# Performance work log

Measured on AMD Instinct MI355X. Metric: run time of the kernel, lower is better.

## Reference

```python
import jax, jax.numpy as jnp
import numpy as np

CH = 512
GROUPS = 32  # _valid_num_groups(512, 32)
EPS = 1e-6

def setup_inputs() -> dict:
    key = jax.random.key(0)
    ks = jax.random.split(key, 11)
    B, C, H, W = 8, CH, 64, 64
    s = 0.02
    return {
        "x": jax.random.normal(ks[0], (B, C, H, W), jnp.float32),
        "gn_w": jnp.ones((C,), jnp.float32),
        "gn_b": jnp.zeros((C,), jnp.float32),
        "q_w": jax.random.normal(ks[1], (C, C), jnp.float32) * s,
        "q_b": jnp.zeros((C,), jnp.float32),
        "k_w": jax.random.normal(ks[2], (C, C), jnp.float32) * s,
        "k_b": jnp.zeros((C,), jnp.float32),
        "v_w": jax.random.normal(ks[3], (C, C), jnp.float32) * s,
        "v_b": jnp.zeros((C,), jnp.float32),
        "proj_w": jax.random.normal(ks[4], (C, C), jnp.float32) * s,
        "proj_b": jnp.zeros((C,), jnp.float32),
    }

def _group_norm(x, w, b):
    B, C, H, W = x.shape
    g = GROUPS
    xg = x.reshape(B, g, C // g, H, W)
    mu = xg.mean(axis=(2, 3, 4), keepdims=True)
    var = xg.var(axis=(2, 3, 4), keepdims=True)
    xn = ((xg - mu) * jax.lax.rsqrt(var + EPS)).reshape(B, C, H, W)
    return xn * w[None, :, None, None] + b[None, :, None, None]

def _conv1x1(h, w, b):
    # h: [B,C,H,W]; w: [Cout,Cin]; 1x1 conv == channel matmul
    return jnp.einsum('bchw,dc->bdhw', h, w) + b[None, :, None, None]

def reference(x, gn_w, gn_b, q_w, q_b, k_w, k_b, v_w, v_b, proj_w, proj_b):
    B, C, H, W = x.shape
    N = H * W
    h = _group_norm(x, gn_w, gn_b)
    q = _conv1x1(h, q_w, q_b).reshape(B, C, N)  # [B,C,N]
    k = _conv1x1(h, k_w, k_b).reshape(B, C, N)
    v = _conv1x1(h, v_w, v_b).reshape(B, C, N)
    # attn[b,i,j] = sum_c q[b,c,i]*k[b,c,j] scaled
    attn = jnp.einsum('bci,bcj->bij', q, k) * (C ** -0.5)
    attn = jax.nn.softmax(attn, axis=-1)
    # out[b,c,i] = sum_j v[b,c,j]*attn[b,i,j]  (bmm(v, attn^T))
    o = jnp.einsum('bcj,bij->bci', v, attn).reshape(B, C, H, W)
    o = _conv1x1(o, proj_w, proj_b)
    return x + o
```

## Files before the change

kernel.cpp:

```cpp
#include <hip/hip_runtime.h>

typedef unsigned short u16;
typedef __attribute__((ext_vector_type(8))) short short8;
typedef __attribute__((ext_vector_type(4))) float f32x4;

__device__ __forceinline__ u16 f32_to_bf16(float f) {
  unsigned u = __float_as_uint(f);
  u += 0x7fffu + ((u >> 16) & 1u);
  return (u16)(u >> 16);
}
__device__ __forceinline__ float bf16_to_f32(u16 h) {
  return __uint_as_float(((unsigned)h) << 16);
}

#define GLD_LDS16(gp, lp)                                                  \
  __builtin_amdgcn_global_load_lds(                                        \
      (const __attribute__((address_space(1))) void*)(gp),                 \
      (__attribute__((address_space(3))) void*)(lp), 16, 0, 0)

#define WAITVM(n) asm volatile("s_waitcnt vmcnt(" #n ")" ::: "memory")

__device__ __forceinline__ void wg_barrier() {
  asm volatile("" ::: "memory");
  __builtin_amdgcn_s_barrier();
  asm volatile("" ::: "memory");
}

__global__ __launch_bounds__(256) void cvt4_f32_bf16(const float* __restrict__ s0,
                                                     const float* __restrict__ s1,
                                                     const float* __restrict__ s2,
                                                     const float* __restrict__ s3,
                                                     u16* __restrict__ d0,
                                                     u16* __restrict__ d1,
                                                     u16* __restrict__ d2,
                                                     u16* __restrict__ d3) {
  const float* s = blockIdx.y == 0 ? s0 : blockIdx.y == 1 ? s1 : blockIdx.y == 2 ? s2 : s3;
  u16* d = blockIdx.y == 0 ? d0 : blockIdx.y == 1 ? d1 : blockIdx.y == 2 ? d2 : d3;
  int i = blockIdx.x * 256 + threadIdx.x;
  float4 v = ((const float4*)s)[i];
  uint2 r;
  r.x = (unsigned)f32_to_bf16(v.x) | ((unsigned)f32_to_bf16(v.y) << 16);
  r.y = (unsigned)f32_to_bf16(v.z) | ((unsigned)f32_to_bf16(v.w) << 16);
  ((uint2*)d)[i] = r;
}

__global__ __launch_bounds__(1024) void gn_stats(const float* __restrict__ x,
                                                 float2* __restrict__ stats) {
  int bg = blockIdx.x;
  const float* xp = x + (long)bg * 65536;
  int t = threadIdx.x;
  float s = 0.f, ss = 0.f;
  for (int i = t; i < 16384; i += 1024) {
    float4 v = ((const float4*)xp)[i];
    s += (v.x + v.y) + (v.z + v.w);
    ss += (v.x * v.x + v.y * v.y) + (v.z * v.z + v.w * v.w);
  }
#pragma unroll
  for (int o = 32; o; o >>= 1) { s += __shfl_xor(s, o); ss += __shfl_xor(ss, o); }
  __shared__ float rs[16], rq[16];
  int wave = t >> 6, lane = t & 63;
  if (lane == 0) { rs[wave] = s; rq[wave] = ss; }
  __syncthreads();
  if (wave == 0) {
    float a = lane < 16 ? rs[lane] : 0.f;
    float b = lane < 16 ? rq[lane] : 0.f;
#pragma unroll
    for (int o = 8; o; o >>= 1) { a += __shfl_xor(a, o); b += __shfl_xor(b, o); }
    if (lane == 0) {
      float mean = a * (1.f / 65536.f);
      float var = b * (1.f / 65536.f) - mean * mean;
      stats[bg] = make_float2(mean, rsqrtf(var + 1e-6f));
    }
  }
}

__global__ __launch_bounds__(256) void gn_apply_t(const float* __restrict__ x,
                                                  const float* __restrict__ gw,
                                                  const float* __restrict__ gb,
                                                  const float2* __restrict__ stats,
                                                  u16* __restrict__ hT) {
  const int g = blockIdx.y, bb = blockIdx.z;
  const float2 st = stats[bb * 32 + g];
  const float mean = st.x, rstd = st.y;
  const float* xp = x + ((long)bb * 512 + g * 16) * 4096;
  u16* hp = hT + (long)bb * 4096 * 512 + g * 16;
  const int i = blockIdx.x * 1024 + threadIdx.x * 4;
#pragma unroll
  for (int half = 0; half < 2; ++half) {
    float w[8], bv[8];
#pragma unroll
    for (int c = 0; c < 8; ++c) {
      w[c] = gw[g * 16 + half * 8 + c] * rstd;
      bv[c] = gb[g * 16 + half * 8 + c];
    }
    float v[8][4];
#pragma unroll
    for (int c = 0; c < 8; ++c) {
      float4 f = *(const float4*)(xp + (long)(half * 8 + c) * 4096 + i);
      v[c][0] = f.x; v[c][1] = f.y; v[c][2] = f.z; v[c][3] = f.w;
    }
#pragma unroll
    for (int p = 0; p < 4; ++p) {
      u16 o[8];
#pragma unroll
      for (int c = 0; c < 8; ++c) o[c] = f32_to_bf16((v[c][p] - mean) * w[c] + bv[c]);
      *(int4*)(hp + (long)(i + p) * 512 + half * 8) = *(int4*)o;
    }
  }
}

template <int BN>
__global__ __launch_bounds__(512, 2) void gemm256(
    const u16* __restrict__ Ab, long sA, int lda,
    const u16* __restrict__ Bb, long sB, int ldb,
    u16* __restrict__ Cb, long sC, int ldc,
    const float* __restrict__ biasM, const float* __restrict__ biasN,
    float scale, int K) {
  constexpr int NFR = BN / 64;
  constexpr int BCH = (BN * 32 * 2) / (512 * 16);
  __shared__ __align__(16) u16 As[4][256 * 32];
  __shared__ __align__(16) u16 Bs[4][BN * 32];
  const u16* A = Ab + (long)blockIdx.z * sA;
  const u16* B = Bb + (long)blockIdx.z * sB;
  const int m0 = blockIdx.y * 256, n0 = blockIdx.x * BN;
  const int t = threadIdx.x;
  const int wave = t >> 6, lane = t & 63;
  const int wy = wave >> 2, wx = wave & 3;
  const int lr = lane & 15, q = lane >> 4;
  const int NT = K >> 5;

  long aoff[2];
  int aldsb[2];
#pragma unroll
  for (int cc = 0; cc < 2; ++cc) {
    int c = cc * 512 + t;
    int row = c >> 2, sl = c & 3;
    int qs = sl ^ ((row >> 1) & 3);
    aoff[cc] = (long)(m0 + row) * lda + qs * 8;
    aldsb[cc] = (cc * 512 + wave * 64) * 8;
  }
  long boff[BCH];
  int bldsb[BCH];
#pragma unroll
  for (int cc = 0; cc < BCH; ++cc) {
    int c = cc * 512 + t;
    int row = c >> 2, sl = c & 3;
    int qs = sl ^ ((row >> 1) & 3);
    boff[cc] = (long)(n0 + row) * ldb + qs * 8;
    bldsb[cc] = (cc * 512 + wave * 64) * 8;
  }

  auto stageA = [&](int tt2) {
    const int bi2 = tt2 & 3;
    const long kk = (long)tt2 << 5;
#pragma unroll
    for (int cc = 0; cc < 2; ++cc) GLD_LDS16(A + aoff[cc] + kk, &As[bi2][aldsb[cc]]);
  };
  auto stageB = [&](int tt2) {
    const int bi2 = tt2 & 3;
    const long kk = (long)tt2 << 5;
#pragma unroll
    for (int cc = 0; cc < BCH; ++cc) GLD_LDS16(B + boff[cc] + kk, &Bs[bi2][bldsb[cc]]);
  };

  const int so = ((q ^ ((lr >> 1) & 3)) << 3);
  const int arow = wy * 128;
  const int brow = wx * (BN / 4);

  f32x4 acc[8][NFR] = {};

  stageA(0); stageB(0); stageA(1); stageB(1); stageA(2); stageB(2);

  for (int tt = 0; tt < NT; ++tt) {
    const int bi = tt & 3;
    if (tt + 3 < NT) stageA(tt + 3);
    const int nf = NT - 1 - tt;
    if (BN == 256) {
      if (nf >= 3) WAITVM(10);
      else if (nf == 2) WAITVM(8);
      else if (nf == 1) WAITVM(4);
      else WAITVM(0);
    } else {
      if (nf >= 3) WAITVM(8);
      else if (nf == 2) WAITVM(6);
      else if (nf == 1) WAITVM(3);
      else WAITVM(0);
    }
    wg_barrier();
    short8 a0[4], bfr[NFR];
#pragma unroll
    for (int i = 0; i < 4; ++i)
      a0[i] = *(const short8*)(&As[bi][0] + (arow + i * 16 + lr) * 32 + so);
#pragma unroll
    for (int j = 0; j < NFR; ++j)
      bfr[j] = *(const short8*)(&Bs[bi][0] + (brow + j * 16 + lr) * 32 + so);
    __builtin_amdgcn_s_setprio(1);
#pragma unroll
    for (int i = 0; i < 4; ++i)
#pragma unroll
      for (int j = 0; j < NFR; ++j)
        acc[i][j] = __builtin_amdgcn_mfma_f32_16x16x32_bf16(a0[i], bfr[j], acc[i][j], 0, 0, 0);
    __builtin_amdgcn_s_setprio(0);
    wg_barrier();
    if (tt + 3 < NT) stageB(tt + 3);
    short8 a1[4];
#pragma unroll
    for (int i = 0; i < 4; ++i)
      a1[i] = *(const short8*)(&As[bi][0] + (arow + 64 + i * 16 + lr) * 32 + so);
    __builtin_amdgcn_s_setprio(1);
#pragma unroll
    for (int i = 0; i < 4; ++i)
#pragma unroll
      for (int j = 0; j < NFR; ++j)
        acc[4 + i][j] = __builtin_amdgcn_mfma_f32_16x16x32_bf16(a1[i], bfr[j], acc[4 + i][j], 0, 0, 0);
    __builtin_amdgcn_s_setprio(0);
    wg_barrier();
  }

#pragma unroll
  for (int i = 0; i < 8; ++i) {
#pragma unroll
    for (int r = 0; r < 4; ++r) {
      const int mr = m0 + wy * 128 + i * 16 + q * 4 + r;
      const float bm = biasM ? biasM[mr] : 0.f;
#pragma unroll
      for (int j = 0; j < NFR; ++j) {
        const int nc = n0 + wx * (BN / 4) + j * 16 + lr;
        float vv = acc[i][j][r] + bm;
        if (biasN) vv += biasN[nc];
        vv *= scale;
        Cb[(long)blockIdx.z * sC + (long)mr * ldc + nc] = f32_to_bf16(vv);
      }
    }
  }
}

template <int EPI>
__global__ __launch_bounds__(256) void gemm128(
    const u16* __restrict__ Ab, long sA, int lda,
    const u16* __restrict__ Bb, long sB, int ldb,
    void* __restrict__ Cb, long sC, int ldc,
    const float* __restrict__ biasM, const float* __restrict__ biasN,
    float scale, const float* __restrict__ res, long sR, int K) {
  const u16* A = Ab + (long)blockIdx.z * sA;
  const u16* B = Bb + (long)blockIdx.z * sB;
  const int m0 = blockIdx.y * 128, n0 = blockIdx.x * 128;
  const int t = threadIdx.x;
  const int wave = t >> 6, lane = t & 63;
  const int wy = wave >> 1, wx = wave & 1;
  const int lr = lane & 15, q = lane >> 4;
  __shared__ __align__(16) u16 As[128 * 32];
  __shared__ __align__(16) u16 Bs[128 * 32];
  f32x4 acc[4][4] = {};
  for (int k0 = 0; k0 < K; k0 += 32) {
#pragma unroll
    for (int c = 0; c < 2; ++c) {
      const int chunk = c * 256 + t;
      const int row = chunk >> 2, ko = (chunk & 3) << 3;
      const int ldsoff = (c * 256 + wave * 64) * 8;
      GLD_LDS16(A + (long)(m0 + row) * lda + (k0 + ko), As + ldsoff);
      GLD_LDS16(B + (long)(n0 + row) * ldb + (k0 + ko), Bs + ldsoff);
    }
    __syncthreads();
    short8 af[4], bf[4];
#pragma unroll
    for (int i = 0; i < 4; ++i)
      af[i] = *(const short8*)(&As[(wy * 64 + i * 16 + lr) * 32 + q * 8]);
#pragma unroll
    for (int j = 0; j < 4; ++j)
      bf[j] = *(const short8*)(&Bs[(wx * 64 + j * 16 + lr) * 32 + q * 8]);
#pragma unroll
    for (int i = 0; i < 4; ++i)
#pragma unroll
      for (int j = 0; j < 4; ++j)
        acc[i][j] = __builtin_amdgcn_mfma_f32_16x16x32_bf16(af[i], bf[j], acc[i][j], 0, 0, 0);
    __syncthreads();
  }
#pragma unroll
  for (int i = 0; i < 4; ++i) {
#pragma unroll
    for (int r = 0; r < 4; ++r) {
      const int mr = m0 + wy * 64 + i * 16 + q * 4 + r;
      const float bm = biasM ? biasM[mr] : 0.f;
#pragma unroll
      for (int j = 0; j < 4; ++j) {
        const int nc = n0 + wx * 64 + j * 16 + lr;
        float vv = acc[i][j][r] + bm;
        if (biasN) vv += biasN[nc];
        vv *= scale;
        const long off = (long)blockIdx.z * sC + (long)mr * ldc + nc;
        if (EPI == 0) {
          ((u16*)Cb)[off] = f32_to_bf16(vv);
        } else {
          ((float*)Cb)[off] = vv + res[(long)blockIdx.z * sR + (long)mr * ldc + nc];
        }
      }
    }
  }
}

__global__ __launch_bounds__(256) void softmax_kernel(u16* __restrict__ P) {
  u16* pr = P + (long)blockIdx.y * 4096 * 4096 + (long)blockIdx.x * 4096;
  int t = threadIdx.x;
  int lane = t & 63, wave = t >> 6;
  int4 d0 = ((const int4*)pr)[t];
  int4 d1 = ((const int4*)pr)[t + 256];
  const u16* p0 = (const u16*)&d0;
  const u16* p1 = (const u16*)&d1;
  float v[16];
#pragma unroll
  for (int j = 0; j < 8; ++j) { v[j] = bf16_to_f32(p0[j]); v[8 + j] = bf16_to_f32(p1[j]); }
  float mx = v[0];
#pragma unroll
  for (int j = 1; j < 16; ++j) mx = fmaxf(mx, v[j]);
#pragma unroll
  for (int o = 32; o; o >>= 1) mx = fmaxf(mx, __shfl_xor(mx, o));
  __shared__ float sm[4];
  __shared__ float ssum[4];
  if (lane == 0) sm[wave] = mx;
  __syncthreads();
  mx = fmaxf(fmaxf(sm[0], sm[1]), fmaxf(sm[2], sm[3]));
  float s = 0.f;
#pragma unroll
  for (int j = 0; j < 16; ++j) { v[j] = __expf(v[j] - mx); s += v[j]; }
#pragma unroll
  for (int o = 32; o; o >>= 1) s += __shfl_xor(s, o);
  if (lane == 0) ssum[wave] = s;
  __syncthreads();
  s = ssum[0] + ssum[1] + ssum[2] + ssum[3];
  float inv = 1.0f / s;
  unsigned r0[4], r1[4];
#pragma unroll
  for (int j = 0; j < 4; ++j) {
    r0[j] = (unsigned)f32_to_bf16(v[2 * j] * inv) | ((unsigned)f32_to_bf16(v[2 * j + 1] * inv) << 16);
    r1[j] = (unsigned)f32_to_bf16(v[8 + 2 * j] * inv) | ((unsigned)f32_to_bf16(v[8 + 2 * j + 1] * inv) << 16);
  }
  ((int4*)pr)[t] = *(int4*)r0;
  ((int4*)pr)[t + 256] = *(int4*)r1;
}

extern "C" void kernel_launch(void* const* d_in, const int* in_sizes, int n_in,
                              void* d_out, int out_size, void* d_ws, size_t ws_size,
                              hipStream_t stream) {
  const float* x = (const float*)d_in[0];
  const float* gn_w = (const float*)d_in[1];
  const float* gn_b = (const float*)d_in[2];
  const float* q_w = (const float*)d_in[3];
  const float* q_b = (const float*)d_in[4];
  const float* k_w = (const float*)d_in[5];
  const float* k_b = (const float*)d_in[6];
  const float* v_w = (const float*)d_in[7];
  const float* v_b = (const float*)d_in[8];
  const float* p_w = (const float*)d_in[9];
  const float* p_b = (const float*)d_in[10];

  char* ws = (char*)d_ws;
  const size_t MB = 1ull << 20;
  u16* wqb = (u16*)(ws + 0);
  u16* wkb = (u16*)(ws + 512 * 1024);
  u16* wvb = (u16*)(ws + 1 * MB);
  u16* wpb = (u16*)(ws + 3 * MB / 2);
  u16* hb = (u16*)(ws + 2 * MB);
  u16* vb = (u16*)(ws + 34 * MB);
  u16* Pb = (u16*)(ws + 66 * MB);
  float2* stats = (float2*)(ws + 66 * MB);
  u16* qb = (u16*)d_out;
  u16* kb = (u16*)d_out + 512L * 4096 * 8;
  u16* ob = hb;

  int NB = 1;
  if (ws_size >= 66 * MB + 8 * 32 * MB) NB = 8;
  else if (ws_size >= 66 * MB + 4 * 32 * MB) NB = 4;
  else if (ws_size >= 66 * MB + 2 * 32 * MB) NB = 2;

  cvt4_f32_bf16<<<dim3(256, 4), 256, 0, stream>>>(q_w, k_w, v_w, p_w, wqb, wkb, wvb, wpb);
  gn_stats<<<256, 1024, 0, stream>>>(x, stats);
  gn_apply_t<<<dim3(4, 32, 8), 256, 0, stream>>>(x, gn_w, gn_b, stats, hb);

  const long sCN = 512L * 4096;
  const long sNN = 4096L * 4096;
  const float scale = 0.04419417382415922f;

  gemm256<256><<<dim3(2, 16, 8), 512, 0, stream>>>(
      hb, sCN, 512, wqb, 0, 512, qb, sCN, 512, nullptr, q_b, scale, 512);
  gemm256<256><<<dim3(2, 16, 8), 512, 0, stream>>>(
      hb, sCN, 512, wkb, 0, 512, kb, sCN, 512, nullptr, k_b, 1.0f, 512);
  gemm256<256><<<dim3(16, 2, 8), 512, 0, stream>>>(
      wvb, 0, 512, hb, sCN, 512, vb, sCN, 4096, v_b, nullptr, 1.0f, 512);

  for (int b0 = 0; b0 < 8; b0 += NB) {
    gemm256<256><<<dim3(16, 16, NB), 512, 0, stream>>>(
        qb + b0 * sCN, sCN, 512, kb + b0 * sCN, sCN, 512, Pb, sNN, 4096,
        nullptr, nullptr, 1.0f, 512);
    softmax_kernel<<<dim3(4096, NB), 256, 0, stream>>>(Pb);
    gemm256<128><<<dim3(4, 16, NB), 512, 0, stream>>>(
        Pb, sNN, 4096, vb + b0 * sCN, sCN, 4096, ob + b0 * sCN, sCN, 512,
        nullptr, nullptr, 1.0f, 4096);
  }

  gemm128<1><<<dim3(32, 4, 8), 256, 0, stream>>>(
      wpb, 0, 512, ob, sCN, 512, (float*)d_out, sCN, 4096, p_b, nullptr, 1.0f,
      x, sCN, 512);
}
```

Before: 968.3 us.

## Fuse softmax into QK epilogue stats and PV operand exponentiation

Drops the standalone softmax pass over the 4096x4096 score matrix. The QK GEMM now emits per-tile row max and sum-exp partials, a small kernel combines them into a row max and inverse sum, and the PV GEMM exponentiates the raw scores as it loads A fragments and scales by the inverse sum in its epilogue. This removes one full read and write of the bf16 score matrix per batch. In exchange it adds exp work inside the PV inner loop, and the PV kernel moves to a 3-deep pipeline with a higher occupancy target, which may add register or LDS pressure.

```diff
diff --git a/kernel.cpp b/kernel.cpp
--- a/kernel.cpp
+++ b/kernel.cpp
@@ -109,17 +109,21 @@
   }
 }
 
-template <int BN>
-__global__ __launch_bounds__(512, 2) void gemm256(
+template <int BN, int MODE>
+__global__ __launch_bounds__(512, MODE == 2 ? 4 : 2) void gemm256(
     const u16* __restrict__ Ab, long sA, int lda,
     const u16* __restrict__ Bb, long sB, int ldb,
     u16* __restrict__ Cb, long sC, int ldc,
     const float* __restrict__ biasM, const float* __restrict__ biasN,
-    float scale, int K) {
+    float scale, int K,
+    float2* __restrict__ pstat, const float* __restrict__ MrowP,
+    const float* __restrict__ SinvP) {
   constexpr int NFR = BN / 64;
   constexpr int BCH = (BN * 32 * 2) / (512 * 16);
-  __shared__ __align__(16) u16 As[4][256 * 32];
-  __shared__ __align__(16) u16 Bs[4][BN * 32];
+  constexpr int DEPTH = (MODE == 2 ? 3 : 4);
+  constexpr int AHEAD = DEPTH - 1;
+  __shared__ __align__(16) u16 As[DEPTH][256 * 32];
+  __shared__ __align__(16) u16 Bs[DEPTH][BN * 32];
   const u16* A = Ab + (long)blockIdx.z * sA;
   const u16* B = Bb + (long)blockIdx.z * sB;
   const int m0 = blockIdx.y * 256, n0 = blockIdx.x * BN;
@@ -150,50 +154,68 @@
     bldsb[cc] = (cc * 512 + wave * 64) * 8;
   }
 
-  auto stageA = [&](int tt2) {
-    const int bi2 = tt2 & 3;
+  auto stageA = [&](int tt2, int buf) {
     const long kk = (long)tt2 << 5;
 #pragma unroll
-    for (int cc = 0; cc < 2; ++cc) GLD_LDS16(A + aoff[cc] + kk, &As[bi2][aldsb[cc]]);
+    for (int cc = 0; cc < 2; ++cc) GLD_LDS16(A + aoff[cc] + kk, &As[buf][aldsb[cc]]);
   };
-  auto stageB = [&](int tt2) {
-    const int bi2 = tt2 & 3;
+  auto stageB = [&](int tt2, int buf) {
     const long kk = (long)tt2 << 5;
 #pragma unroll
-    for (int cc = 0; cc < BCH; ++cc) GLD_LDS16(B + boff[cc] + kk, &Bs[bi2][bldsb[cc]]);
+    for (int cc = 0; cc < BCH; ++cc) GLD_LDS16(B + boff[cc] + kk, &Bs[buf][bldsb[cc]]);
   };
 
   const int so = ((q ^ ((lr >> 1) & 3)) << 3);
   const int arow = wy * 128;
   const int brow = wx * (BN / 4);
 
+  float mrow[8];
+  if (MODE == 2) {
+#pragma unroll
+    for (int i = 0; i < 4; ++i) {
+      mrow[i] = MrowP[(long)blockIdx.z * 4096 + m0 + arow + i * 16 + lr];
+      mrow[4 + i] = MrowP[(long)blockIdx.z * 4096 + m0 + arow + 64 + i * 16 + lr];
+    }
+  }
+
   f32x4 acc[8][NFR] = {};
 
-  stageA(0); stageB(0); stageA(1); stageB(1); stageA(2); stageB(2);
-
+#pragma unroll
+  for (int pt = 0; pt < AHEAD; ++pt) { stageA(pt, pt); stageB(pt, pt); }
+
+  int bcur = 0;
   for (int tt = 0; tt < NT; ++tt) {
-    const int bi = tt & 3;
-    if (tt + 3 < NT) stageA(tt + 3);
+    const int bst = (bcur == 0) ? DEPTH - 1 : bcur - 1;
+    if (tt + AHEAD < NT) stageA(tt + AHEAD, bst);
     const int nf = NT - 1 - tt;
-    if (BN == 256) {
+    if (MODE == 2) {
+      if (nf >= 2) WAITVM(5);
+      else if (nf == 1) WAITVM(3);
+      else WAITVM(0);
+    } else {
       if (nf >= 3) WAITVM(10);
       else if (nf == 2) WAITVM(8);
       else if (nf == 1) WAITVM(4);
       else WAITVM(0);
-    } else {
-      if (nf >= 3) WAITVM(8);
-      else if (nf == 2) WAITVM(6);
-      else if (nf == 1) WAITVM(3);
-      else WAITVM(0);
     }
     wg_barrier();
     short8 a0[4], bfr[NFR];
 #pragma unroll
     for (int i = 0; i < 4; ++i)
-      a0[i] = *(const short8*)(&As[bi][0] + (arow + i * 16 + lr) * 32 + so);
+      a0[i] = *(const short8*)(&As[bcur][0] + (arow + i * 16 + lr) * 32 + so);
 #pragma unroll
     for (int j = 0; j < NFR; ++j)
-      bfr[j] = *(const short8*)(&Bs[bi][0] + (brow + j * 16 + lr) * 32 + so);
+      bfr[j] = *(const short8*)(&Bs[bcur][0] + (brow + j * 16 + lr) * 32 + so);
+    if (MODE == 2) {
+#pragma unroll
+      for (int i = 0; i < 4; ++i) {
+        short8 o;
+#pragma unroll
+        for (int e = 0; e < 8; ++e)
+          o[e] = (short)f32_to_bf16(__expf(bf16_to_f32((u16)a0[i][e]) - mrow[i]));
+        a0[i] = o;
+      }
+    }
     __builtin_amdgcn_s_setprio(1);
 #pragma unroll
     for (int i = 0; i < 4; ++i)
@@ -202,11 +224,21 @@
         acc[i][j] = __builtin_amdgcn_mfma_f32_16x16x32_bf16(a0[i], bfr[j], acc[i][j], 0, 0, 0);
     __builtin_amdgcn_s_setprio(0);
     wg_barrier();
-    if (tt + 3 < NT) stageB(tt + 3);
+    if (tt + AHEAD < NT) stageB(tt + AHEAD, bst);
     short8 a1[4];
 #pragma unroll
     for (int i = 0; i < 4; ++i)
-      a1[i] = *(const short8*)(&As[bi][0] + (arow + 64 + i * 16 + lr) * 32 + so);
+      a1[i] = *(const short8*)(&As[bcur][0] + (arow + 64 + i * 16 + lr) * 32 + so);
+    if (MODE == 2) {
+#pragma unroll
+      for (int i = 0; i < 4; ++i) {
+        short8 o;
+#pragma unroll
+        for (int e = 0; e < 8; ++e)
+          o[e] = (short)f32_to_bf16(__expf(bf16_to_f32((u16)a1[i][e]) - mrow[4 + i]));
+        a1[i] = o;
+      }
+    }
     __builtin_amdgcn_s_setprio(1);
 #pragma unroll
     for (int i = 0; i < 4; ++i)
@@ -215,6 +247,70 @@
         acc[4 + i][j] = __builtin_amdgcn_mfma_f32_16x16x32_bf16(a1[i], bfr[j], acc[4 + i][j], 0, 0, 0);
     __builtin_amdgcn_s_setprio(0);
     wg_barrier();
+    bcur = (bcur + 1 == DEPTH) ? 0 : bcur + 1;
+  }
+
+  if (MODE == 1) {
+    float* sredM = (float*)&As[0][0];
+    float* sredS = sredM + 4 * 256;
+    float pm[8][4], ps[8][4];
+#pragma unroll
+    for (int i = 0; i < 8; ++i)
+#pragma unroll
+      for (int r = 0; r < 4; ++r) {
+        float m = acc[i][0][r];
+#pragma unroll
+        for (int j = 1; j < NFR; ++j) m = fmaxf(m, acc[i][j][r]);
+#pragma unroll
+        for (int o = 1; o < 16; o <<= 1) m = fmaxf(m, __shfl_xor(m, o));
+        pm[i][r] = m;
+      }
+    if (lr == 0) {
+#pragma unroll
+      for (int i = 0; i < 8; ++i)
+#pragma unroll
+        for (int r = 0; r < 4; ++r)
+          sredM[wx * 256 + wy * 128 + i * 16 + q * 4 + r] = pm[i][r];
+    }
+    __syncthreads();
+#pragma unroll
+    for (int i = 0; i < 8; ++i)
+#pragma unroll
+      for (int r = 0; r < 4; ++r) {
+        const int row = wy * 128 + i * 16 + q * 4 + r;
+        pm[i][r] = fmaxf(fmaxf(sredM[row], sredM[256 + row]),
+                         fmaxf(sredM[512 + row], sredM[768 + row]));
+      }
+#pragma unroll
+    for (int i = 0; i < 8; ++i)
+#pragma unroll
+      for (int r = 0; r < 4; ++r) {
+        float s = 0.f;
+#pragma unroll
+        for (int j = 0; j < NFR; ++j) s += __expf(acc[i][j][r] - pm[i][r]);
+#pragma unroll
+        for (int o = 1; o < 16; o <<= 1) s += __shfl_xor(s, o);
+        ps[i][r] = s;
+      }
+    if (lr == 0) {
+#pragma unroll
+      for (int i = 0; i < 8; ++i)
+#pragma unroll
+        for (int r = 0; r < 4; ++r)
+          sredS[wx * 256 + wy * 128 + i * 16 + q * 4 + r] = ps[i][r];
+    }
+    __syncthreads();
+    if (lr == 0 && wx == 0) {
+#pragma unroll
+      for (int i = 0; i < 8; ++i)
+#pragma unroll
+        for (int r = 0; r < 4; ++r) {
+          const int row = wy * 128 + i * 16 + q * 4 + r;
+          const float S = sredS[row] + sredS[256 + row] + sredS[512 + row] + sredS[768 + row];
+          pstat[((long)blockIdx.z * 16 + blockIdx.x) * 4096 + (m0 + row)] =
+              make_float2(pm[i][r], S);
+        }
+    }
   }
 
 #pragma unroll
@@ -222,17 +318,43 @@
 #pragma unroll
     for (int r = 0; r < 4; ++r) {
       const int mr = m0 + wy * 128 + i * 16 + q * 4 + r;
-      const float bm = biasM ? biasM[mr] : 0.f;
+      float rowmul = 1.f, rowadd = 0.f;
+      if (MODE == 2) rowmul = SinvP[(long)blockIdx.z * 4096 + mr];
+      else if (biasM) rowadd = biasM[mr];
 #pragma unroll
       for (int j = 0; j < NFR; ++j) {
         const int nc = n0 + wx * (BN / 4) + j * 16 + lr;
-        float vv = acc[i][j][r] + bm;
-        if (biasN) vv += biasN[nc];
-        vv *= scale;
+        float vv = acc[i][j][r];
+        if (MODE == 2) {
+          vv *= rowmul;
+        } else {
+          vv += rowadd;
+          if (biasN) vv += biasN[nc];
+          vv *= scale;
+        }
         Cb[(long)blockIdx.z * sC + (long)mr * ldc + nc] = f32_to_bf16(vv);
       }
     }
   }
+}
+
+__global__ __launch_bounds__(256) void combine_stats(const float2* __restrict__ ps,
+                                                     float* __restrict__ Mrow,
+                                                     float* __restrict__ Sinv) {
+  const int row = blockIdx.x * 256 + threadIdx.x;
+  const long z = blockIdx.y;
+  const float2* p = ps + z * 16 * 4096 + row;
+  float m = p[0].x;
+#pragma unroll
+  for (int i = 1; i < 16; ++i) m = fmaxf(m, p[(long)i * 4096].x);
+  float s = 0.f;
+#pragma unroll
+  for (int i = 0; i < 16; ++i) {
+    float2 v = p[(long)i * 4096];
+    s += v.y * __expf(v.x - m);
+  }
+  Mrow[z * 4096 + row] = m;
+  Sinv[z * 4096 + row] = 1.0f / s;
 }
 
 template <int EPI>
@@ -299,46 +421,6 @@
   }
 }
 
-__global__ __launch_bounds__(256) void softmax_kernel(u16* __restrict__ P) {
-  u16* pr = P + (long)blockIdx.y * 4096 * 4096 + (long)blockIdx.x * 4096;
-  int t = threadIdx.x;
-  int lane = t & 63, wave = t >> 6;
-  int4 d0 = ((const int4*)pr)[t];
-  int4 d1 = ((const int4*)pr)[t + 256];
-  const u16* p0 = (const u16*)&d0;
-  const u16* p1 = (const u16*)&d1;
-  float v[16];
-#pragma unroll
-  for (int j = 0; j < 8; ++j) { v[j] = bf16_to_f32(p0[j]); v[8 + j] = bf16_to_f32(p1[j]); }
-  float mx = v[0];
-#pragma unroll
-  for (int j = 1; j < 16; ++j) mx = fmaxf(mx, v[j]);
-#pragma unroll
-  for (int o = 32; o; o >>= 1) mx = fmaxf(mx, __shfl_xor(mx, o));
-  __shared__ float sm[4];
-  __shared__ float ssum[4];
-  if (lane == 0) sm[wave] = mx;
-  __syncthreads();
-  mx = fmaxf(fmaxf(sm[0], sm[1]), fmaxf(sm[2], sm[3]));
-  float s = 0.f;
-#pragma unroll
-  for (int j = 0; j < 16; ++j) { v[j] = __expf(v[j] - mx); s += v[j]; }
-#pragma unroll
-  for (int o = 32; o; o >>= 1) s += __shfl_xor(s, o);
-  if (lane == 0) ssum[wave] = s;
-  __syncthreads();
-  s = ssum[0] + ssum[1] + ssum[2] + ssum[3];
-  float inv = 1.0f / s;
-  unsigned r0[4], r1[4];
-#pragma unroll
-  for (int j = 0; j < 4; ++j) {
-    r0[j] = (unsigned)f32_to_bf16(v[2 * j] * inv) | ((unsigned)f32_to_bf16(v[2 * j + 1] * inv) << 16);
-    r1[j] = (unsigned)f32_to_bf16(v[8 + 2 * j] * inv) | ((unsigned)f32_to_bf16(v[8 + 2 * j + 1] * inv) << 16);
-  }
-  ((int4*)pr)[t] = *(int4*)r0;
-  ((int4*)pr)[t + 256] = *(int4*)r1;
-}
-
 extern "C" void kernel_launch(void* const* d_in, const int* in_sizes, int n_in,
                               void* d_out, int out_size, void* d_ws, size_t ws_size,
                               hipStream_t stream) {
@@ -363,39 +445,46 @@
   u16* hb = (u16*)(ws + 2 * MB);
   u16* vb = (u16*)(ws + 34 * MB);
   u16* Pb = (u16*)(ws + 66 * MB);
-  float2* stats = (float2*)(ws + 66 * MB);
+  float2* gnstats = (float2*)(ws + 66 * MB);
   u16* qb = (u16*)d_out;
   u16* kb = (u16*)d_out + 512L * 4096 * 8;
   u16* ob = hb;
 
   int NB = 1;
-  if (ws_size >= 66 * MB + 8 * 32 * MB) NB = 8;
-  else if (ws_size >= 66 * MB + 4 * 32 * MB) NB = 4;
-  else if (ws_size >= 66 * MB + 2 * 32 * MB) NB = 2;
+  if (ws_size >= (66 + 8 * 32 + 5) * MB) NB = 8;
+  else if (ws_size >= (66 + 4 * 32 + 5) * MB) NB = 4;
+  else if (ws_size >= (66 + 2 * 32 + 5) * MB) NB = 2;
+
+  float2* pstat = (float2*)(ws + 66 * MB + (size_t)NB * 32 * MB);
+  float* Mr = (float*)(pstat + (size_t)NB * 16 * 4096);
+  float* Si = Mr + (size_t)NB * 4096;
 
   cvt4_f32_bf16<<<dim3(256, 4), 256, 0, stream>>>(q_w, k_w, v_w, p_w, wqb, wkb, wvb, wpb);
-  gn_stats<<<256, 1024, 0, stream>>>(x, stats);
-  gn_apply_t<<<dim3(4, 32, 8), 256, 0, stream>>>(x, gn_w, gn_b, stats, hb);
+  gn_stats<<<256, 1024, 0, stream>>>(x, gnstats);
+  gn_apply_t<<<dim3(4, 32, 8), 256, 0, stream>>>(x, gn_w, gn_b, gnstats, hb);
 
   const long sCN = 512L * 4096;
   const long sNN = 4096L * 4096;
   const float scale = 0.04419417382415922f;
 
-  gemm256<256><<<dim3(2, 16, 8), 512, 0, stream>>>(
-      hb, sCN, 512, wqb, 0, 512, qb, sCN, 512, nullptr, q_b, scale, 512);
-  gemm256<256><<<dim3(2, 16, 8), 512, 0, stream>>>(
-      hb, sCN, 512, wkb, 0, 512, kb, sCN, 512, nullptr, k_b, 1.0f, 512);
-  gemm256<256><<<dim3(16, 2, 8), 512, 0, stream>>>(
-      wvb, 0, 512, hb, sCN, 512, vb, sCN, 4096, v_b, nullptr, 1.0f, 512);
+  gemm256<256, 0><<<dim3(2, 16, 8), 512, 0, stream>>>(
+      hb, sCN, 512, wqb, 0, 512, qb, sCN, 512, nullptr, q_b, scale, 512,
+      nullptr, nullptr, nullptr);
+  gemm256<256, 0><<<dim3(2, 16, 8), 512, 0, stream>>>(
+      hb, sCN, 512, wkb, 0, 512, kb, sCN, 512, nullptr, k_b, 1.0f, 512,
+      nullptr, nullptr, nullptr);
+  gemm256<256, 0><<<dim3(16, 2, 8), 512, 0, stream>>>(
+      wvb, 0, 512, hb, sCN, 512, vb, sCN, 4096, v_b, nullptr, 1.0f, 512,
+      nullptr, nullptr, nullptr);
 
   for (int b0 = 0; b0 < 8; b0 += NB) {
-    gemm256<256><<<dim3(16, 16, NB), 512, 0, stream>>>(
+    gemm256<256, 1><<<dim3(16, 16, NB), 512, 0, stream>>>(
         qb + b0 * sCN, sCN, 512, kb + b0 * sCN, sCN, 512, Pb, sNN, 4096,
-        nullptr, nullptr, 1.0f, 512);
-    softmax_kernel<<<dim3(4096, NB), 256, 0, stream>>>(Pb);
-    gemm256<128><<<dim3(4, 16, NB), 512, 0, stream>>>(
+        nullptr, nullptr, 1.0f, 512, pstat, nullptr, nullptr);
+    combine_stats<<<dim3(16, NB), 256, 0, stream>>>(pstat, Mr, Si);
+    gemm256<128, 2><<<dim3(4, 16, NB), 512, 0, stream>>>(
         Pb, sNN, 4096, vb + b0 * sCN, sCN, 4096, ob + b0 * sCN, sCN, 512,
-        nullptr, nullptr, 1.0f, 4096);
+        nullptr, nullptr, 1.0f, 4096, nullptr, Mr, Si);
   }
 
   gemm128<1><<<dim3(32, 4, 8), 256, 0, stream>>>(
```

New measurement: 1.453 ms. +50.0%, slower.
